# Kernel optimization log

Measured on AMD Instinct MI355X. Metric: run time of the kernel, lower is better.

Reference implementation:

```python
import jax, jax.numpy as jnp
import numpy as np

NSLC, NPC, ETL, NCHA = 2, 3, 4, 4
NX = NY = 128
NLIN, NCOL = 128, 256


def golden_angle_traj(nlin, ncol):
    ga = np.pi * (3.0 - np.sqrt(5.0))  # golden angle
    kr = np.linspace(-np.pi, np.pi, ncol, endpoint=False)  # readout coords
    th = ga * np.arange(nlin)
    kx = np.cos(th)[:, None] * kr[None, :]
    ky = np.sin(th)[:, None] * kr[None, :]
    return np.stack([kx, ky], axis=-1).astype(np.float32)  # [nlin, ncol, 2]


def setup_inputs() -> dict:
    key = jax.random.key(0)
    ks = jax.random.split(key, 5)
    return {
        "image_re": jax.random.normal(ks[0], (NSLC, NPC, NX, NY), jnp.float32),
        "image_im": jax.random.normal(ks[1], (NSLC, NPC, NX, NY), jnp.float32),
        "smaps_re": jax.random.normal(ks[2], (NSLC, NCHA, NX, NY), jnp.float32),
        "smaps_im": jax.random.normal(ks[3], (NSLC, NCHA, NX, NY), jnp.float32),
        "D": jax.random.normal(ks[4], (NSLC, ETL, NPC), jnp.float32),
        "mask": jnp.ones((NSLC, NLIN, NCOL), jnp.float32),
        "traj": jnp.asarray(golden_angle_traj(NLIN, NCOL)),
    }


def reference(image_re, image_im, smaps_re, smaps_im, D, mask, traj):
    image = (image_re + 1j * image_im).astype(jnp.complex64)  # [s, p, x, y]
    smaps = (smaps_re + 1j * smaps_im).astype(jnp.complex64)  # [s, c, x, y]
    nslc, npc, nx, ny = image.shape
    ncha = smaps.shape[1]
    etl = D.shape[-2]
    nlin, ncol = traj.shape[0], traj.shape[1]
    nlin_pe = nlin // etl

    # PC2Contrast: mix principal-component images into etl contrast images
    img = jnp.einsum('sep,spxy->sexy', D.astype(jnp.complex64), image)
    # coil images per contrast: [s, c, e, x, y]
    coil = img[:, None, :, :, :] * smaps[:, :, None, :, :]

    xs = (jnp.arange(nx) - nx // 2).astype(jnp.float32)
    ys = (jnp.arange(ny) - ny // 2).astype(jnp.float32)
    traj_e = traj.reshape(etl, nlin_pe, ncol, 2)  # echo-major line grouping

    ks = []
    for ee in range(etl):  # fixed small echo-train loop
        kx = traj_e[ee, :, :, 0].reshape(-1)  # [M]
        ky = traj_e[ee, :, :, 1].reshape(-1)
        Ey = jnp.exp(-1j * ky[:, None] * ys[None, :])  # [M, ny] c64
        Ex = jnp.exp(-1j * kx[:, None] * xs[None, :])  # [M, nx] c64
        c = coil[:, :, ee].reshape(nslc * ncha, nx, ny)
        T = jnp.einsum('bxy,my->bmx', c, Ey)          # y-contraction
        k = jnp.einsum('bmx,mx->bm', T, Ex)           # x-phase reduction
        ks.append(k.reshape(nslc, ncha, nlin_pe, ncol))
    kspace = jnp.concatenate(ks, axis=2).astype(jnp.complex64)  # [s,c,nlin,ncol]

    kspace = kspace * mask[:, None, :, :].astype(jnp.complex64)
    # return real/imag stacked so the harness stays in real dtypes
    return jnp.stack([kspace.real, kspace.imag], axis=-1)
```

## Files before the change

kernel.cpp:

```cpp
#include <hip/hip_runtime.h>
#include <math.h>

#define NSLC 2
#define NPC 3
#define ETL 4
#define NCHA 4
#define NX 128
#define NY 128
#define NLIN 128
#define NCOL 256
#define NLIN_PE 32
#define NB 8
#define NROW 1024
#define NTILE 64

typedef __attribute__((ext_vector_type(8))) short short8;
typedef __attribute__((ext_vector_type(4))) float float4_t;

static __device__ __forceinline__ unsigned short f2bf(float f) {
  unsigned u = __float_as_uint(f);
  unsigned r = (u + 0x7FFFu + ((u >> 16) & 1u)) >> 16;
  return (unsigned short)r;
}

__global__ __launch_bounds__(256) void prep_coil(
    const float* __restrict__ imR, const float* __restrict__ imI,
    const float* __restrict__ smR, const float* __restrict__ smI,
    const float* __restrict__ Dm, unsigned short* __restrict__ A) {
  int tid = blockIdx.x * blockDim.x + threadIdx.x;
  if (tid >= NSLC * NX * NY) return;
  int y = tid & (NY - 1);
  int x = (tid >> 7) & (NX - 1);
  int s = tid >> 14;

  float ir[NPC], ii[NPC];
#pragma unroll
  for (int p = 0; p < NPC; ++p) {
    int idx = ((s * NPC + p) * NX + x) * NY + y;
    ir[p] = imR[idx];
    ii[p] = imI[idx];
  }
  float sr[NCHA], si[NCHA];
#pragma unroll
  for (int c = 0; c < NCHA; ++c) {
    int idx = ((s * NCHA + c) * NX + x) * NY + y;
    sr[c] = smR[idx];
    si[c] = smI[idx];
  }
#pragma unroll
  for (int e = 0; e < ETL; ++e) {
    float gr = 0.f, gi = 0.f;
#pragma unroll
    for (int p = 0; p < NPC; ++p) {
      float d = Dm[(s * ETL + e) * NPC + p];
      gr += d * ir[p];
      gi += d * ii[p];
    }
#pragma unroll
    for (int c = 0; c < NCHA; ++c) {
      int row = (s * NCHA + c) * NX + x;
      int rt = row >> 4;
      float cr = gr * sr[c] - gi * si[c];
      float ci = gr * si[c] + gi * sr[c];
      unsigned short* dst = A + (e * NTILE + rt) * 4096 + (row & 15) * 8 + (y & 7);
      dst[(y >> 3) * 128] = f2bf(cr);
      dst[(16 + (y >> 3)) * 128] = f2bf(ci);
    }
  }
}

__global__ __launch_bounds__(256) void radtse_mfma(
    const unsigned short* __restrict__ A, const float* __restrict__ traj,
    const float* __restrict__ mask, float* __restrict__ out) {
  __shared__ __align__(16) char lds[65536];

  const int tid = threadIdx.x;
  const int w = tid >> 6;
  const int lane = tid & 63;
  const int e = blockIdx.x >> 9;
  const int m0 = (blockIdx.x & 511) << 4;
  const int lin = e * NLIN_PE + (m0 >> 8);

  {
    const int m = tid & 15;
    const int g0 = (tid >> 4) * 2;
    const int col = (m0 + m) & (NCOL - 1);
    const float ky = traj[(lin * NCOL + col) * 2 + 1];
#pragma unroll
    for (int gg = 0; gg < 2; ++gg) {
      const int g = g0 + gg;
      short8 vr, vi;
#pragma unroll
      for (int j = 0; j < 8; ++j) {
        const int k = g * 8 + j;
        float sn, cs;
        __sincosf(ky * (float)((k & 127) - 64), &sn, &cs);
        vr[j] = (short)f2bf((k < 128) ? cs : sn);
        vi[j] = (short)f2bf((k < 128) ? -sn : cs);
      }
      *(short8*)(lds + g * 256 + m * 16) = vr;
      *(short8*)(lds + 8192 + g * 256 + m * 16) = vi;
    }
  }

  const int mloc = lane & 15;
  const int xsub = lane >> 4;
  float exr[2][4], exi[2][4];
  {
    const int col = (m0 + mloc) & (NCOL - 1);
    const float kx = traj[(lin * NCOL + col) * 2 + 0];
#pragma unroll
    for (int par = 0; par < 2; ++par) {
      const int xb = (w + par * 4) * 16 + xsub * 4;
#pragma unroll
      for (int r = 0; r < 4; ++r) {
        float sn, cs;
        __sincosf(kx * (float)(xb + r - 64), &sn, &cs);
        exr[par][r] = cs;
        exi[par][r] = -sn;
      }
    }
  }
  __syncthreads();

  short8 bfr[2][8];
#pragma unroll
  for (int ct = 0; ct < 2; ++ct)
#pragma unroll
    for (int kk = 0; kk < 8; ++kk)
      bfr[ct][kk] = *(const short8*)(lds + ct * 8192 + kk * 1024 + lane * 16);
  __syncthreads();

  float kr[8], ki[8];
#pragma unroll
  for (int b = 0; b < 8; ++b) {
    kr[b] = 0.f;
    ki[b] = 0.f;
  }

  const unsigned short* Ae = A + e * (NTILE * 4096);
  char* Abuf = lds + w * 16384;

  {
    const unsigned short* src = Ae + w * 4096 + lane * 8;
#pragma unroll
    for (int j = 0; j < 8; ++j)
      __builtin_amdgcn_global_load_lds(
          (const __attribute__((address_space(1))) unsigned int*)(src + j * 512),
          (__attribute__((address_space(3))) unsigned int*)(Abuf + j * 1024), 16,
          0, 0);
  }

#pragma unroll
  for (int i = 0; i < 16; ++i) {
    const int b = i >> 1;
    const int par = i & 1;

    if (i < 15) {
      asm volatile("s_waitcnt lgkmcnt(0)" ::: "memory");
      const int rt = w + (i + 1) * 4;
      const unsigned short* src = Ae + rt * 4096 + lane * 8;
      char* dstb = Abuf + ((i + 1) & 1) * 8192;
#pragma unroll
      for (int j = 0; j < 8; ++j)
        __builtin_amdgcn_global_load_lds(
            (const __attribute__((address_space(1))) unsigned int*)(src + j * 512),
            (__attribute__((address_space(3))) unsigned int*)(dstb + j * 1024),
            16, 0, 0);
      asm volatile("s_waitcnt vmcnt(8)" ::: "memory");
    } else {
      asm volatile("s_waitcnt vmcnt(0)" ::: "memory");
    }

    const char* abase = Abuf + (i & 1) * 8192 + lane * 16;
    short8 afr[8];
#pragma unroll
    for (int kk = 0; kk < 8; ++kk)
      afr[kk] = *(const short8*)(abase + kk * 1024);

    float4_t accR = {0.f, 0.f, 0.f, 0.f};
    float4_t accI = {0.f, 0.f, 0.f, 0.f};
#pragma unroll
    for (int kk = 0; kk < 8; ++kk) {
      accR = __builtin_amdgcn_mfma_f32_16x16x32_bf16(afr[kk], bfr[0][kk], accR,
                                                     0, 0, 0);
      accI = __builtin_amdgcn_mfma_f32_16x16x32_bf16(afr[kk], bfr[1][kk], accI,
                                                     0, 0, 0);
    }
#pragma unroll
    for (int r = 0; r < 4; ++r) {
      const float xr = exr[par][r];
      const float xi = exi[par][r];
      kr[b] += accR[r] * xr - accI[r] * xi;
      ki[b] += accR[r] * xi + accI[r] * xr;
    }
  }

  __syncthreads();
  float* comb = (float*)lds;
#pragma unroll
  for (int b = 0; b < 8; ++b) {
    float r = kr[b], im = ki[b];
    r += __shfl_xor(r, 16, 64);
    r += __shfl_xor(r, 32, 64);
    im += __shfl_xor(im, 16, 64);
    im += __shfl_xor(im, 32, 64);
    if (lane < 16) {
      comb[((w * 16 + lane) * 8 + b) * 2 + 0] = r;
      comb[((w * 16 + lane) * 8 + b) * 2 + 1] = im;
    }
  }
  __syncthreads();
  {
    const int m_l = tid >> 4;
    const int b = (tid >> 1) & 7;
    const int ri = tid & 1;
    float v = 0.f;
#pragma unroll
    for (int ww = 0; ww < 4; ++ww) v += comb[((ww * 16 + m_l) * 8 + b) * 2 + ri];
    const int m = m0 + m_l;
    const int col = m & (NCOL - 1);
    const int s = b >> 2;
    const float mv = mask[(s * NLIN + lin) * NCOL + col];
    out[((b * NLIN + lin) * NCOL + col) * 2 + ri] = v * mv;
  }
}

extern "C" void kernel_launch(void* const* d_in, const int* in_sizes, int n_in,
                              void* d_out, int out_size, void* d_ws, size_t ws_size,
                              hipStream_t stream) {
  const float* imR = (const float*)d_in[0];
  const float* imI = (const float*)d_in[1];
  const float* smR = (const float*)d_in[2];
  const float* smI = (const float*)d_in[3];
  const float* Dm = (const float*)d_in[4];
  const float* mask = (const float*)d_in[5];
  const float* traj = (const float*)d_in[6];
  float* out = (float*)d_out;
  unsigned short* A = (unsigned short*)d_ws;

  prep_coil<<<dim3(NSLC * NX * NY / 256), dim3(256), 0, stream>>>(imR, imI, smR,
                                                                  smI, Dm, A);
  radtse_mfma<<<dim3(ETL * 512), dim3(256), 0, stream>>>(A, traj, mask, out);
}
```

Baseline: 65.65 us.

## Process two k-space groups per block and give each wave its own coil batches

Each block now handles 32 k-space samples in two 16-sample groups. The A tiles staged in LDS are reused for both groups, which halves global and LDS traffic for A per sample. Each wave owns two whole coil/slice batches, so the cross-wave LDS reduction and its barriers go away. The y-phase B fragments are built directly in registers instead of going through LDS. The x-phase factors are advanced with a complex rotation recurrence instead of a fresh sincos per step. The cost is higher register pressure, with launch bounds set to one block, and half as many blocks in the grid.

```diff
diff --git a/kernel.cpp b/kernel.cpp
--- a/kernel.cpp
+++ b/kernel.cpp
@@ -11,11 +11,13 @@
 #define NCOL 256
 #define NLIN_PE 32
 #define NB 8
-#define NROW 1024
 #define NTILE 64
 
 typedef __attribute__((ext_vector_type(8))) short short8;
 typedef __attribute__((ext_vector_type(4))) float float4_t;
+
+#define AS1 __attribute__((address_space(1)))
+#define AS3 __attribute__((address_space(3)))
 
 static __device__ __forceinline__ unsigned short f2bf(float f) {
   unsigned u = __float_as_uint(f);
@@ -69,7 +71,7 @@
   }
 }
 
-__global__ __launch_bounds__(256) void radtse_mfma(
+__global__ __launch_bounds__(256, 1) void radtse_mfma(
     const unsigned short* __restrict__ A, const float* __restrict__ traj,
     const float* __restrict__ mask, float* __restrict__ out) {
   __shared__ __align__(16) char lds[65536];
@@ -77,152 +79,159 @@
   const int tid = threadIdx.x;
   const int w = tid >> 6;
   const int lane = tid & 63;
-  const int e = blockIdx.x >> 9;
-  const int m0 = (blockIdx.x & 511) << 4;
+  const int e = blockIdx.x >> 8;
+  const int m0 = (blockIdx.x & 255) << 5;
   const int lin = e * NLIN_PE + (m0 >> 8);
-
-  {
-    const int m = tid & 15;
-    const int g0 = (tid >> 4) * 2;
-    const int col = (m0 + m) & (NCOL - 1);
-    const float ky = traj[(lin * NCOL + col) * 2 + 1];
-#pragma unroll
-    for (int gg = 0; gg < 2; ++gg) {
-      const int g = g0 + gg;
+  const int mloc = lane & 15;
+  const int ksl = lane >> 4;
+
+  float kyv[2], kxv[2];
+#pragma unroll
+  for (int mg = 0; mg < 2; ++mg) {
+    const int col = (m0 + mg * 16 + mloc) & (NCOL - 1);
+    kxv[mg] = traj[(lin * NCOL + col) * 2 + 0];
+    kyv[mg] = traj[(lin * NCOL + col) * 2 + 1];
+  }
+
+  short8 bfr[2][2][8];
+#pragma unroll
+  for (int mg = 0; mg < 2; ++mg) {
+#pragma unroll
+    for (int kk = 0; kk < 8; ++kk) {
       short8 vr, vi;
 #pragma unroll
       for (int j = 0; j < 8; ++j) {
-        const int k = g * 8 + j;
+        const int k = kk * 32 + ksl * 8 + j;
         float sn, cs;
-        __sincosf(ky * (float)((k & 127) - 64), &sn, &cs);
-        vr[j] = (short)f2bf((k < 128) ? cs : sn);
-        vi[j] = (short)f2bf((k < 128) ? -sn : cs);
-      }
-      *(short8*)(lds + g * 256 + m * 16) = vr;
-      *(short8*)(lds + 8192 + g * 256 + m * 16) = vi;
-    }
-  }
-
-  const int mloc = lane & 15;
-  const int xsub = lane >> 4;
-  float exr[2][4], exi[2][4];
-  {
-    const int col = (m0 + mloc) & (NCOL - 1);
-    const float kx = traj[(lin * NCOL + col) * 2 + 0];
-#pragma unroll
-    for (int par = 0; par < 2; ++par) {
-      const int xb = (w + par * 4) * 16 + xsub * 4;
-#pragma unroll
-      for (int r = 0; r < 4; ++r) {
-        float sn, cs;
-        __sincosf(kx * (float)(xb + r - 64), &sn, &cs);
-        exr[par][r] = cs;
-        exi[par][r] = -sn;
-      }
-    }
-  }
-  __syncthreads();
-
-  short8 bfr[2][8];
-#pragma unroll
-  for (int ct = 0; ct < 2; ++ct)
-#pragma unroll
-    for (int kk = 0; kk < 8; ++kk)
-      bfr[ct][kk] = *(const short8*)(lds + ct * 8192 + kk * 1024 + lane * 16);
-  __syncthreads();
-
-  float kr[8], ki[8];
-#pragma unroll
-  for (int b = 0; b < 8; ++b) {
-    kr[b] = 0.f;
-    ki[b] = 0.f;
-  }
-
-  const unsigned short* Ae = A + e * (NTILE * 4096);
-  char* Abuf = lds + w * 16384;
-
-  {
-    const unsigned short* src = Ae + w * 4096 + lane * 8;
+        __sincosf(kyv[mg] * (float)((k & 127) - 64), &sn, &cs);
+        vr[j] = (short)f2bf(k < 128 ? cs : sn);
+        vi[j] = (short)f2bf(k < 128 ? -sn : cs);
+      }
+      bfr[mg][0][kk] = vr;
+      bfr[mg][1][kk] = vi;
+    }
+  }
+
+  float exr[2][4], exi[2][4], str[2], sti[2];
+#pragma unroll
+  for (int mg = 0; mg < 2; ++mg) {
+#pragma unroll
+    for (int r = 0; r < 4; ++r) {
+      float sn, cs;
+      __sincosf(kxv[mg] * (float)(ksl * 4 + r - 64), &sn, &cs);
+      exr[mg][r] = cs;
+      exi[mg][r] = -sn;
+    }
+    float sn, cs;
+    __sincosf(kxv[mg] * 16.0f, &sn, &cs);
+    str[mg] = cs;
+    sti[mg] = -sn;
+  }
+
+  float kr[2][2], ki[2][2];
+#pragma unroll
+  for (int mg = 0; mg < 2; ++mg)
+#pragma unroll
+    for (int bl = 0; bl < 2; ++bl) {
+      kr[mg][bl] = 0.f;
+      ki[mg][bl] = 0.f;
+    }
+
+  const char* Ae = (const char*)(A + e * (NTILE * 4096));
+  char* mybuf = lds + w * 16384;
+
+  auto STAGE = [&](int i) {
+    const char* src = Ae + (w * 16 + i) * 8192 + lane * 16;
+    char* d = mybuf + (i & 1) * 8192;
 #pragma unroll
     for (int j = 0; j < 8; ++j)
-      __builtin_amdgcn_global_load_lds(
-          (const __attribute__((address_space(1))) unsigned int*)(src + j * 512),
-          (__attribute__((address_space(3))) unsigned int*)(Abuf + j * 1024), 16,
-          0, 0);
-  }
+      __builtin_amdgcn_global_load_lds((const AS1 unsigned int*)(src + j * 1024),
+                                       (AS3 unsigned int*)(d + j * 1024), 16, 0,
+                                       0);
+  };
+
+  STAGE(0);
 
 #pragma unroll
   for (int i = 0; i < 16; ++i) {
-    const int b = i >> 1;
-    const int par = i & 1;
-
+    const int bl = i >> 3;
+    asm volatile("s_waitcnt lgkmcnt(0)" ::: "memory");
     if (i < 15) {
-      asm volatile("s_waitcnt lgkmcnt(0)" ::: "memory");
-      const int rt = w + (i + 1) * 4;
-      const unsigned short* src = Ae + rt * 4096 + lane * 8;
-      char* dstb = Abuf + ((i + 1) & 1) * 8192;
-#pragma unroll
-      for (int j = 0; j < 8; ++j)
-        __builtin_amdgcn_global_load_lds(
-            (const __attribute__((address_space(1))) unsigned int*)(src + j * 512),
-            (__attribute__((address_space(3))) unsigned int*)(dstb + j * 1024),
-            16, 0, 0);
+      STAGE(i + 1);
       asm volatile("s_waitcnt vmcnt(8)" ::: "memory");
     } else {
       asm volatile("s_waitcnt vmcnt(0)" ::: "memory");
     }
 
-    const char* abase = Abuf + (i & 1) * 8192 + lane * 16;
+    const char* ab = mybuf + (i & 1) * 8192 + ksl * 256 + mloc * 16;
     short8 afr[8];
 #pragma unroll
     for (int kk = 0; kk < 8; ++kk)
-      afr[kk] = *(const short8*)(abase + kk * 1024);
-
-    float4_t accR = {0.f, 0.f, 0.f, 0.f};
-    float4_t accI = {0.f, 0.f, 0.f, 0.f};
-#pragma unroll
-    for (int kk = 0; kk < 8; ++kk) {
-      accR = __builtin_amdgcn_mfma_f32_16x16x32_bf16(afr[kk], bfr[0][kk], accR,
-                                                     0, 0, 0);
-      accI = __builtin_amdgcn_mfma_f32_16x16x32_bf16(afr[kk], bfr[1][kk], accI,
-                                                     0, 0, 0);
-    }
-#pragma unroll
-    for (int r = 0; r < 4; ++r) {
-      const float xr = exr[par][r];
-      const float xi = exi[par][r];
-      kr[b] += accR[r] * xr - accI[r] * xi;
-      ki[b] += accR[r] * xi + accI[r] * xr;
-    }
-  }
-
-  __syncthreads();
-  float* comb = (float*)lds;
-#pragma unroll
-  for (int b = 0; b < 8; ++b) {
-    float r = kr[b], im = ki[b];
-    r += __shfl_xor(r, 16, 64);
-    r += __shfl_xor(r, 32, 64);
-    im += __shfl_xor(im, 16, 64);
-    im += __shfl_xor(im, 32, 64);
-    if (lane < 16) {
-      comb[((w * 16 + lane) * 8 + b) * 2 + 0] = r;
-      comb[((w * 16 + lane) * 8 + b) * 2 + 1] = im;
-    }
-  }
-  __syncthreads();
-  {
-    const int m_l = tid >> 4;
-    const int b = (tid >> 1) & 7;
-    const int ri = tid & 1;
-    float v = 0.f;
-#pragma unroll
-    for (int ww = 0; ww < 4; ++ww) v += comb[((ww * 16 + m_l) * 8 + b) * 2 + ri];
-    const int m = m0 + m_l;
-    const int col = m & (NCOL - 1);
-    const int s = b >> 2;
-    const float mv = mask[(s * NLIN + lin) * NCOL + col];
-    out[((b * NLIN + lin) * NCOL + col) * 2 + ri] = v * mv;
+      afr[kk] = *(const short8*)(ab + kk * 1024);
+
+#pragma unroll
+    for (int mg = 0; mg < 2; ++mg) {
+      float4_t aR = {0.f, 0.f, 0.f, 0.f};
+      float4_t aI = {0.f, 0.f, 0.f, 0.f};
+#pragma unroll
+      for (int kk = 0; kk < 8; ++kk) {
+        aR = __builtin_amdgcn_mfma_f32_16x16x32_bf16(afr[kk], bfr[mg][0][kk],
+                                                     aR, 0, 0, 0);
+        aI = __builtin_amdgcn_mfma_f32_16x16x32_bf16(afr[kk], bfr[mg][1][kk],
+                                                     aI, 0, 0, 0);
+      }
+#pragma unroll
+      for (int r = 0; r < 4; ++r) {
+        kr[mg][bl] += aR[r] * exr[mg][r] - aI[r] * exi[mg][r];
+        ki[mg][bl] += aR[r] * exi[mg][r] + aI[r] * exr[mg][r];
+      }
+    }
+
+    if (i == 7) {
+#pragma unroll
+      for (int mg = 0; mg < 2; ++mg)
+#pragma unroll
+        for (int r = 0; r < 4; ++r) {
+          float sn, cs;
+          __sincosf(kxv[mg] * (float)(ksl * 4 + r - 64), &sn, &cs);
+          exr[mg][r] = cs;
+          exi[mg][r] = -sn;
+        }
+    } else if (i < 15) {
+#pragma unroll
+      for (int mg = 0; mg < 2; ++mg)
+#pragma unroll
+        for (int r = 0; r < 4; ++r) {
+          float nr = exr[mg][r] * str[mg] - exi[mg][r] * sti[mg];
+          exi[mg][r] = exr[mg][r] * sti[mg] + exi[mg][r] * str[mg];
+          exr[mg][r] = nr;
+        }
+    }
+  }
+
+#pragma unroll
+  for (int mg = 0; mg < 2; ++mg)
+#pragma unroll
+    for (int bl = 0; bl < 2; ++bl) {
+      kr[mg][bl] += __shfl_xor(kr[mg][bl], 16, 64);
+      kr[mg][bl] += __shfl_xor(kr[mg][bl], 32, 64);
+      ki[mg][bl] += __shfl_xor(ki[mg][bl], 16, 64);
+      ki[mg][bl] += __shfl_xor(ki[mg][bl], 32, 64);
+    }
+
+  if (lane < 16) {
+#pragma unroll
+    for (int mg = 0; mg < 2; ++mg) {
+      const int col = (m0 + mg * 16 + lane) & (NCOL - 1);
+#pragma unroll
+      for (int bl = 0; bl < 2; ++bl) {
+        const int b = 2 * w + bl;
+        const int s = b >> 2;
+        const float mv = mask[(s * NLIN + lin) * NCOL + col];
+        float2 o = make_float2(kr[mg][bl] * mv, ki[mg][bl] * mv);
+        *(float2*)(out + (((b * NLIN) + lin) * NCOL + col) * 2) = o;
+      }
+    }
   }
 }
 
@@ -241,5 +250,5 @@
 
   prep_coil<<<dim3(NSLC * NX * NY / 256), dim3(256), 0, stream>>>(imR, imI, smR,
                                                                   smI, Dm, A);
-  radtse_mfma<<<dim3(ETL * 512), dim3(256), 0, stream>>>(A, traj, mask, out);
-}
+  radtse_mfma<<<dim3(ETL * 256), dim3(256), 0, stream>>>(A, traj, mask, out);
+}
```

New measurement: 78.84 us. +20.1%, slower.

## Build Ey fragments in registers and triple-buffer A tiles at higher occupancy

Applied to the files above, without the earlier changes.

Each lane now computes its own bf16 Ey fragments directly in registers instead of staging them through LDS. It exploits the fact that the imaginary twiddle block is the real block with its cos/sin halves swapped, which halves the B-fragment register set; the complex product is recovered from three accumulators. The A staging changes from a double buffer of full tiles to a three-slot ring of half-tiles, which shrinks LDS to 48KB and allows launch bounds of 3 blocks per CU. The aim is more latency hiding and fewer LDS round trips and barriers in the prologue, at the cost of more waitcnt bookkeeping and redundant sincos work per lane.

```diff
diff --git a/kernel.cpp b/kernel.cpp
--- a/kernel.cpp
+++ b/kernel.cpp
@@ -11,11 +11,13 @@
 #define NCOL 256
 #define NLIN_PE 32
 #define NB 8
-#define NROW 1024
 #define NTILE 64
 
 typedef __attribute__((ext_vector_type(8))) short short8;
 typedef __attribute__((ext_vector_type(4))) float float4_t;
+
+#define AS1 __attribute__((address_space(1)))
+#define AS3 __attribute__((address_space(3)))
 
 static __device__ __forceinline__ unsigned short f2bf(float f) {
   unsigned u = __float_as_uint(f);
@@ -69,10 +71,10 @@
   }
 }
 
-__global__ __launch_bounds__(256) void radtse_mfma(
+__global__ __launch_bounds__(256, 3) void radtse_mfma(
     const unsigned short* __restrict__ A, const float* __restrict__ traj,
     const float* __restrict__ mask, float* __restrict__ out) {
-  __shared__ __align__(16) char lds[65536];
+  __shared__ __align__(16) char lds[49152];
 
   const int tid = threadIdx.x;
   const int w = tid >> 6;
@@ -80,56 +82,39 @@
   const int e = blockIdx.x >> 9;
   const int m0 = (blockIdx.x & 511) << 4;
   const int lin = e * NLIN_PE + (m0 >> 8);
-
-  {
-    const int m = tid & 15;
-    const int g0 = (tid >> 4) * 2;
-    const int col = (m0 + m) & (NCOL - 1);
-    const float ky = traj[(lin * NCOL + col) * 2 + 1];
-#pragma unroll
-    for (int gg = 0; gg < 2; ++gg) {
-      const int g = g0 + gg;
-      short8 vr, vi;
-#pragma unroll
-      for (int j = 0; j < 8; ++j) {
-        const int k = g * 8 + j;
-        float sn, cs;
-        __sincosf(ky * (float)((k & 127) - 64), &sn, &cs);
-        vr[j] = (short)f2bf((k < 128) ? cs : sn);
-        vi[j] = (short)f2bf((k < 128) ? -sn : cs);
-      }
-      *(short8*)(lds + g * 256 + m * 16) = vr;
-      *(short8*)(lds + 8192 + g * 256 + m * 16) = vi;
-    }
-  }
-
   const int mloc = lane & 15;
-  const int xsub = lane >> 4;
+  const int ksl = lane >> 4;
+
+  const int col = (m0 + mloc) & (NCOL - 1);
+  const float kx = traj[(lin * NCOL + col) * 2 + 0];
+  const float ky = traj[(lin * NCOL + col) * 2 + 1];
+
+  short8 bfr[8];
+#pragma unroll
+  for (int kk = 0; kk < 8; ++kk) {
+    short8 v;
+#pragma unroll
+    for (int j = 0; j < 8; ++j) {
+      const int k = kk * 32 + ksl * 8 + j;
+      float sn, cs;
+      __sincosf(ky * (float)((k & 127) - 64), &sn, &cs);
+      v[j] = (short)f2bf(k < 128 ? cs : sn);
+    }
+    bfr[kk] = v;
+  }
+
   float exr[2][4], exi[2][4];
-  {
-    const int col = (m0 + mloc) & (NCOL - 1);
-    const float kx = traj[(lin * NCOL + col) * 2 + 0];
-#pragma unroll
-    for (int par = 0; par < 2; ++par) {
-      const int xb = (w + par * 4) * 16 + xsub * 4;
-#pragma unroll
-      for (int r = 0; r < 4; ++r) {
-        float sn, cs;
-        __sincosf(kx * (float)(xb + r - 64), &sn, &cs);
-        exr[par][r] = cs;
-        exi[par][r] = -sn;
-      }
-    }
-  }
-  __syncthreads();
-
-  short8 bfr[2][8];
-#pragma unroll
-  for (int ct = 0; ct < 2; ++ct)
-#pragma unroll
-    for (int kk = 0; kk < 8; ++kk)
-      bfr[ct][kk] = *(const short8*)(lds + ct * 8192 + kk * 1024 + lane * 16);
-  __syncthreads();
+#pragma unroll
+  for (int par = 0; par < 2; ++par) {
+    const int xb = (w + par * 4) * 16 + ksl * 4;
+#pragma unroll
+    for (int r = 0; r < 4; ++r) {
+      float sn, cs;
+      __sincosf(kx * (float)(xb + r - 64), &sn, &cs);
+      exr[par][r] = cs;
+      exi[par][r] = -sn;
+    }
+  }
 
   float kr[8], ki[8];
 #pragma unroll
@@ -138,76 +123,95 @@
     ki[b] = 0.f;
   }
 
-  const unsigned short* Ae = A + e * (NTILE * 4096);
-  char* Abuf = lds + w * 16384;
-
-  {
-    const unsigned short* src = Ae + w * 4096 + lane * 8;
-#pragma unroll
-    for (int j = 0; j < 8; ++j)
-      __builtin_amdgcn_global_load_lds(
-          (const __attribute__((address_space(1))) unsigned int*)(src + j * 512),
-          (__attribute__((address_space(3))) unsigned int*)(Abuf + j * 1024), 16,
-          0, 0);
-  }
+  const char* Ae = (const char*)(A + e * (NTILE * 4096));
+  char* mybuf = lds + w * 12288;
+
+  auto STAGE = [&](int c) {
+    const int rt = w + (c >> 1) * 4;
+    const char* src = Ae + rt * 8192 + (c & 1) * 4096 + lane * 16;
+    char* d = mybuf + (c % 3) * 4096;
+#pragma unroll
+    for (int j = 0; j < 4; ++j)
+      __builtin_amdgcn_global_load_lds((const AS1 unsigned int*)(src + j * 1024),
+                                       (AS3 unsigned int*)(d + j * 1024), 16, 0,
+                                       0);
+  };
+
+  STAGE(0);
+  STAGE(1);
 
 #pragma unroll
   for (int i = 0; i < 16; ++i) {
     const int b = i >> 1;
     const int par = i & 1;
 
-    if (i < 15) {
+    float4_t accR = {0.f, 0.f, 0.f, 0.f};
+    float4_t accU = {0.f, 0.f, 0.f, 0.f};
+    float4_t accV = {0.f, 0.f, 0.f, 0.f};
+
+#pragma unroll
+    for (int h = 0; h < 2; ++h) {
+      const int c = 2 * i + h;
       asm volatile("s_waitcnt lgkmcnt(0)" ::: "memory");
-      const int rt = w + (i + 1) * 4;
-      const unsigned short* src = Ae + rt * 4096 + lane * 8;
-      char* dstb = Abuf + ((i + 1) & 1) * 8192;
-#pragma unroll
-      for (int j = 0; j < 8; ++j)
-        __builtin_amdgcn_global_load_lds(
-            (const __attribute__((address_space(1))) unsigned int*)(src + j * 512),
-            (__attribute__((address_space(3))) unsigned int*)(dstb + j * 1024),
-            16, 0, 0);
-      asm volatile("s_waitcnt vmcnt(8)" ::: "memory");
-    } else {
-      asm volatile("s_waitcnt vmcnt(0)" ::: "memory");
-    }
-
-    const char* abase = Abuf + (i & 1) * 8192 + lane * 16;
-    short8 afr[8];
-#pragma unroll
-    for (int kk = 0; kk < 8; ++kk)
-      afr[kk] = *(const short8*)(abase + kk * 1024);
-
-    float4_t accR = {0.f, 0.f, 0.f, 0.f};
-    float4_t accI = {0.f, 0.f, 0.f, 0.f};
-#pragma unroll
-    for (int kk = 0; kk < 8; ++kk) {
-      accR = __builtin_amdgcn_mfma_f32_16x16x32_bf16(afr[kk], bfr[0][kk], accR,
-                                                     0, 0, 0);
-      accI = __builtin_amdgcn_mfma_f32_16x16x32_bf16(afr[kk], bfr[1][kk], accI,
-                                                     0, 0, 0);
-    }
+      if (c + 2 < 32) {
+        STAGE(c + 2);
+        asm volatile("s_waitcnt vmcnt(8)" ::: "memory");
+      } else if (c == 30) {
+        asm volatile("s_waitcnt vmcnt(4)" ::: "memory");
+      } else {
+        asm volatile("s_waitcnt vmcnt(0)" ::: "memory");
+      }
+
+      const char* ab = mybuf + (c % 3) * 4096 + ksl * 256 + mloc * 16;
+      short8 afr[4];
+#pragma unroll
+      for (int kk = 0; kk < 4; ++kk)
+        afr[kk] = *(const short8*)(ab + kk * 1024);
+
+      if (h == 0) {
+#pragma unroll
+        for (int kk = 0; kk < 4; ++kk) {
+          accR = __builtin_amdgcn_mfma_f32_16x16x32_bf16(afr[kk], bfr[kk], accR,
+                                                         0, 0, 0);
+          accU = __builtin_amdgcn_mfma_f32_16x16x32_bf16(afr[kk], bfr[kk + 4],
+                                                         accU, 0, 0, 0);
+        }
+      } else {
+#pragma unroll
+        for (int kk = 0; kk < 4; ++kk) {
+          accR = __builtin_amdgcn_mfma_f32_16x16x32_bf16(afr[kk], bfr[kk + 4],
+                                                         accR, 0, 0, 0);
+          accV = __builtin_amdgcn_mfma_f32_16x16x32_bf16(afr[kk], bfr[kk], accV,
+                                                         0, 0, 0);
+        }
+      }
+    }
+
 #pragma unroll
     for (int r = 0; r < 4; ++r) {
-      const float xr = exr[par][r];
-      const float xi = exi[par][r];
-      kr[b] += accR[r] * xr - accI[r] * xi;
-      ki[b] += accR[r] * xi + accI[r] * xr;
-    }
-  }
-
+      const float tr = accR[r];
+      const float ti = accV[r] - accU[r];
+      kr[b] += tr * exr[par][r] - ti * exi[par][r];
+      ki[b] += tr * exi[par][r] + ti * exr[par][r];
+    }
+  }
+
+#pragma unroll
+  for (int b = 0; b < 8; ++b) {
+    kr[b] += __shfl_xor(kr[b], 16, 64);
+    kr[b] += __shfl_xor(kr[b], 32, 64);
+    ki[b] += __shfl_xor(ki[b], 16, 64);
+    ki[b] += __shfl_xor(ki[b], 32, 64);
+  }
+
+  asm volatile("s_waitcnt vmcnt(0) lgkmcnt(0)" ::: "memory");
   __syncthreads();
   float* comb = (float*)lds;
 #pragma unroll
   for (int b = 0; b < 8; ++b) {
-    float r = kr[b], im = ki[b];
-    r += __shfl_xor(r, 16, 64);
-    r += __shfl_xor(r, 32, 64);
-    im += __shfl_xor(im, 16, 64);
-    im += __shfl_xor(im, 32, 64);
     if (lane < 16) {
-      comb[((w * 16 + lane) * 8 + b) * 2 + 0] = r;
-      comb[((w * 16 + lane) * 8 + b) * 2 + 1] = im;
+      comb[((w * 16 + lane) * 8 + b) * 2 + 0] = kr[b];
+      comb[((w * 16 + lane) * 8 + b) * 2 + 1] = ki[b];
     }
   }
   __syncthreads();
@@ -218,11 +222,10 @@
     float v = 0.f;
 #pragma unroll
     for (int ww = 0; ww < 4; ++ww) v += comb[((ww * 16 + m_l) * 8 + b) * 2 + ri];
-    const int m = m0 + m_l;
-    const int col = m & (NCOL - 1);
+    const int colw = (m0 + m_l) & (NCOL - 1);
     const int s = b >> 2;
-    const float mv = mask[(s * NLIN + lin) * NCOL + col];
-    out[((b * NLIN + lin) * NCOL + col) * 2 + ri] = v * mv;
+    const float mv = mask[(s * NLIN + lin) * NCOL + colw];
+    out[((b * NLIN + lin) * NCOL + colw) * 2 + ri] = v * mv;
   }
 }
 
```

After: 100.5 us. 53.0% more time.
